# Kernel tuning notes

Hardware: AMD Instinct MI355X
Metric: run time of the kernel (lower is better)

Reference implementation:

```python
import jax, jax.numpy as jnp
import numpy as np

V, D, N, K = 500000, 64, 50000, 32


def setup_inputs() -> dict:
    key = jax.random.key(0)
    ks = jax.random.split(key, 8)
    return {
        "embeddings": jax.random.normal(ks[0], (V, D), dtype=jnp.float32),
        "W1": jax.random.normal(ks[1], (2 * D, D), dtype=jnp.float32) * 0.05,
        "b1": jnp.zeros((D,), dtype=jnp.float32),
        "W2": jax.random.normal(ks[2], (D, D), dtype=jnp.float32) * 0.05,
        "b2": jnp.zeros((D,), dtype=jnp.float32),
        "w3": jax.random.normal(ks[3], (D, 1), dtype=jnp.float32) * 0.05,
        "b3": jnp.zeros((1,), dtype=jnp.float32),
        "video_nodes": jax.random.randint(ks[4], (N,), 0, V, dtype=jnp.int32),
        "neigh_idx": jax.random.randint(ks[5], (N, K), 0, V, dtype=jnp.int32),
        "neigh_deg": jax.random.randint(ks[6], (N,), 0, K + 1, dtype=jnp.int32),
    }


def reference(embeddings, W1, b1, W2, b2, w3, b3, video_nodes, neigh_idx, neigh_deg):
    # Ragged neighbor gather (padded to K, masked by degree)
    e = embeddings[neigh_idx]                      # [N, K, D] neighbor embeddings
    u = embeddings[video_nodes]                    # [N, D]    center embeddings
    # GraphRec-style attention: MLP on [neigh, center] concat -> scalar score
    x = jnp.concatenate(
        [e, jnp.broadcast_to(u[:, None, :], e.shape)], axis=-1)  # [N, K, 2D]
    h = jax.nn.relu(x @ W1 + b1)
    h = jax.nn.relu(h @ W2 + b2)
    s = (h @ w3)[..., 0] + b3[0]                   # [N, K]
    mask = jnp.arange(K)[None, :] < neigh_deg[:, None]
    s = jnp.where(mask, s, -1e9)                   # mask padded neighbors
    att = jax.nn.softmax(s, axis=-1)               # softmax over valid neighbors
    out = jnp.einsum('nkd,nk->nd', e, att)         # attention-weighted sum
    # num_neighs == 0 -> fall back to node's own embedding
    out = jnp.where((neigh_deg > 0)[:, None], out, u)
    return out
```

## Files before the change

kernel.cpp:

```cpp
#include <hip/hip_runtime.h>
#include <hip/hip_bf16.h>

typedef __bf16 bf16x8 __attribute__((ext_vector_type(8)));
typedef float  f32x4  __attribute__((ext_vector_type(4)));

#define MFMA32(acc, a, b) acc = __builtin_amdgcn_mfma_f32_16x16x32_bf16(a, b, acc, 0, 0, 0)
#define LD4(p) (*(const float4*)(p))

__device__ __forceinline__ bf16x8 cvt8(float4 a, float4 b) {
  bf16x8 r;
  r[0] = (__bf16)a.x; r[1] = (__bf16)a.y; r[2] = (__bf16)a.z; r[3] = (__bf16)a.w;
  r[4] = (__bf16)b.x; r[5] = (__bf16)b.y; r[6] = (__bf16)b.z; r[7] = (__bf16)b.w;
  return r;
}

template <int CTRL>
__device__ __forceinline__ float dpp_mov(float x) {
  int yi = __builtin_amdgcn_update_dpp(0, __builtin_bit_cast(int, x), CTRL, 0xF, 0xF, true);
  return __builtin_bit_cast(float, yi);
}
template <int CTRL>
__device__ __forceinline__ float dpp_fadd(float x) { return x + dpp_mov<CTRL>(x); }
template <int CTRL>
__device__ __forceinline__ float dpp_fmax(float x) { return fmaxf(x, dpp_mov<CTRL>(x)); }

__device__ __forceinline__ float tree16(const float* o, int lr) {
  float q8[8];
#pragma unroll
  for (int t = 0; t < 8; t++) {
    const bool up = (lr & 8);
    float sel = up ? o[t + 8] : o[t];
    float oth = up ? o[t] : o[t + 8];
    q8[t] = sel + dpp_mov<0x128>(oth);
  }
  float q4[4];
#pragma unroll
  for (int t = 0; t < 4; t++) {
    const bool up = (lr & 4);
    float sel = up ? q8[t + 4] : q8[t];
    float oth = up ? q8[t] : q8[t + 4];
    q4[t] = sel + __shfl_xor(oth, 4);
  }
  float q2[2];
#pragma unroll
  for (int t = 0; t < 2; t++) {
    const bool up = (lr & 2);
    float sel = up ? q4[t + 2] : q4[t];
    float oth = up ? q4[t] : q4[t + 2];
    q2[t] = sel + dpp_mov<0x4E>(oth);
  }
  const bool up = (lr & 1);
  float sel = up ? q2[1] : q2[0];
  float oth = up ? q2[0] : q2[1];
  return sel + dpp_mov<0xB1>(oth);
}

__global__ void prep_frags(const float* __restrict__ W1,
                           const float* __restrict__ W2,
                           __bf16* __restrict__ wf) {
  int idx = blockIdx.x * 256 + threadIdx.x;
  if (idx < 8192) {
    int j = idx & 7, lane = (idx >> 3) & 63, mt = (idx >> 9) & 3, ks = idx >> 11;
    int i = ks * 32 + ((lane >> 4) << 3) + j;
    int col = mt * 16 + (lane & 15);
    wf[idx] = (__bf16)W1[i * 64 + col];
  } else if (idx < 12288) {
    int t = idx - 8192;
    int j = t & 7, lane = (t >> 3) & 63, mt2 = (t >> 9) & 3, ks2 = (t >> 11) & 1;
    int g = (lane >> 4) & 3;
    int rho = (ks2 * 2 + (j >> 2)) * 16 + g * 4 + (j & 3);
    wf[idx] = (__bf16)W2[rho * 64 + mt2 * 16 + (lane & 15)];
  }
}

__global__ __launch_bounds__(512) void graph_agg(
    const float* __restrict__ emb,
    const float* __restrict__ b1g, const float* __restrict__ b2g,
    const float* __restrict__ w3g, const float* __restrict__ b3g,
    const int* __restrict__ vn, const int* __restrict__ ni,
    const int* __restrict__ nd,
    const __bf16* __restrict__ wf,
    float* __restrict__ out, int N) {
  __shared__ __align__(16) unsigned char smem[25344];

  {
    const uint4* src = (const uint4*)wf;
    uint4* dst = (uint4*)smem;
#pragma unroll
    for (int i = 0; i < 3; i++) dst[threadIdx.x + i * 512] = src[threadIdx.x + i * 512];
    int t = threadIdx.x;
    if (t < 64) {
      ((float*)(smem + 24576))[t] = b1g[t];
      ((float*)(smem + 24832))[t] = b2g[t];
      ((float*)(smem + 25088))[t] = w3g[t];
    }
  }
  __syncthreads();

  const __bf16* w1f = (const __bf16*)smem;
  const __bf16* w2f = (const __bf16*)(smem + 16384);
  const int wid = threadIdx.x >> 6;
  const int l   = threadIdx.x & 63;
  const int g   = l >> 4;
  const int lr  = l & 15;
  const float b3v = b3g[0];

  const int gw = blockIdx.x * 8 + wid;
  const int nwaves = gridDim.x * 8;

  int n = gw;
  int node = 0, deg = 0, i0 = 0, i1 = 0;
  if (n < N) {
    node = vn[n]; deg = nd[n];
    i0 = ni[(long)n * 32 + lr]; i1 = ni[(long)n * 32 + 16 + lr];
  }

  for (; n < N; n += nwaves) {
    const int cn = node, cd = deg, ci0 = i0, ci1 = i1;
    {
      int nn = n + nwaves; if (nn >= N) nn = n;
      node = vn[nn]; deg = nd[nn];
      i0 = ni[(long)nn * 32 + lr]; i1 = ni[(long)nn * 32 + 16 + lr];
    }
    const float* ub = emb + (long)cn * 64;

    if (cd == 0) {
      out[(long)n * 64 + l] = ub[l];
      continue;
    }
    const bool m1 = (cd > 16);

    int boff = 24576;
    asm volatile("" : "+v"(boff));
    const unsigned char* bb = smem + boff;

    bf16x8 ef00, ef01, ef10, ef11;
    {
      const int a = (lr < cd) ? ci0 : cn;
      const float* p = emb + (long)a * 64 + g * 8;
      ef00 = cvt8(LD4(p), LD4(p + 4));
      ef01 = cvt8(LD4(p + 32), LD4(p + 36));
    }
    if (m1) {
      const int a = (16 + lr < cd) ? ci1 : cn;
      const float* p = emb + (long)a * 64 + g * 8;
      ef10 = cvt8(LD4(p), LD4(p + 4));
      ef11 = cvt8(LD4(p + 32), LD4(p + 36));
    }
    bf16x8 uf0, uf1;
    {
      const float* q = ub + g * 8;
      uf0 = cvt8(LD4(q), LD4(q + 4));
      uf1 = cvt8(LD4(q + 32), LD4(q + 36));
    }

    auto mlp_pass = [&](bf16x8 EFa, bf16x8 EFb) -> float {
      f32x4 acc[4];
#pragma unroll
      for (int mt = 0; mt < 4; mt++)
        acc[mt] = *(const f32x4*)(bb + (mt * 16 + g * 4) * 4);
      const bf16x8 xbs[4] = {EFa, EFb, uf0, uf1};
#pragma unroll
      for (int ks = 0; ks < 4; ks++) {
#pragma unroll
        for (int mt = 0; mt < 4; mt++) {
          bf16x8 wa = *(const bf16x8*)(w1f + ((ks * 4 + mt) * 64 + l) * 8);
          MFMA32(acc[mt], wa, xbs[ks]);
        }
      }
      bf16x8 hb[2];
#pragma unroll
      for (int ks2 = 0; ks2 < 2; ks2++) {
        bf16x8 v;
#pragma unroll
        for (int j = 0; j < 8; j++) {
          const int mt = ks2 * 2 + (j >> 2), r = j & 3;
          v[j] = (__bf16)fmaxf(acc[mt][r], 0.f);
        }
        hb[ks2] = v;
      }
#pragma unroll
      for (int mt2 = 0; mt2 < 4; mt2++)
        acc[mt2] = *(const f32x4*)(bb + 256 + (mt2 * 16 + g * 4) * 4);
#pragma unroll
      for (int ks2 = 0; ks2 < 2; ks2++) {
#pragma unroll
        for (int mt2 = 0; mt2 < 4; mt2++) {
          bf16x8 wa = *(const bf16x8*)(w2f + ((ks2 * 4 + mt2) * 64 + l) * 8);
          MFMA32(acc[mt2], wa, hb[ks2]);
        }
      }
      float sv = 0.f;
#pragma unroll
      for (int mt2 = 0; mt2 < 4; mt2++) {
        f32x4 wv = *(const f32x4*)(bb + 512 + (mt2 * 16 + g * 4) * 4);
#pragma unroll
        for (int r = 0; r < 4; r++)
          sv += fmaxf(acc[mt2][r], 0.f) * wv[r];
      }
      sv += __shfl_xor(sv, 16);
      sv += __shfl_xor(sv, 32);
      return sv;
    };

    float sv0 = mlp_pass(ef00, ef01);
    float sv1 = m1 ? mlp_pass(ef10, ef11) : 0.f;

    const bool v0 = (lr < cd);
    const bool v1 = m1 && (16 + lr < cd);
    sv0 = v0 ? (sv0 + b3v) : -1e30f;
    sv1 = v1 ? (sv1 + b3v) : -1e30f;

    float mx = fmaxf(sv0, sv1);
    mx = dpp_fmax<0x128>(mx);
    mx = dpp_fmax<0x124>(mx);
    mx = dpp_fmax<0x122>(mx);
    mx = dpp_fmax<0x121>(mx);

    float p0 = v0 ? __expf(sv0 - mx) : 0.f;
    float p1 = v1 ? __expf(sv1 - mx) : 0.f;
    float sum = p0 + p1;
    sum = dpp_fadd<0x128>(sum);
    sum = dpp_fadd<0x124>(sum);
    sum = dpp_fadd<0x122>(sum);
    sum = dpp_fadd<0x121>(sum);
    const float inv = 1.f / sum;
    const float a0 = p0 * inv, a1 = p1 * inv;

    float o[16];
#pragma unroll
    for (int j = 0; j < 8; j++) {
      float v = a0 * (float)ef00[j];
      if (m1) v += a1 * (float)ef10[j];
      o[j] = v;
      float w = a0 * (float)ef01[j];
      if (m1) w += a1 * (float)ef11[j];
      o[8 + j] = w;
    }
    const int dim = ((lr >> 3) << 5) + g * 8 + (lr & 7);
    out[(long)n * 64 + dim] = tree16(o, lr);
  }
}

extern "C" void kernel_launch(void* const* d_in, const int* in_sizes, int n_in,
                              void* d_out, int out_size, void* d_ws, size_t ws_size,
                              hipStream_t stream) {
  const float* emb = (const float*)d_in[0];
  const float* W1  = (const float*)d_in[1];
  const float* b1  = (const float*)d_in[2];
  const float* W2  = (const float*)d_in[3];
  const float* b2  = (const float*)d_in[4];
  const float* w3  = (const float*)d_in[5];
  const float* b3  = (const float*)d_in[6];
  const int* vn = (const int*)d_in[7];
  const int* ni = (const int*)d_in[8];
  const int* nd = (const int*)d_in[9];
  float* out = (float*)d_out;
  const int N = in_sizes[7];
  __bf16* wf = (__bf16*)d_ws;

  prep_frags<<<48, 256, 0, stream>>>(W1, W2, wf);
  graph_agg<<<2048, 512, 0, stream>>>(emb, b1, b2, w3, b3, vn, ni, nd, wf, out, N);
}
```

Measured before the change: 92.75 us.

## Split each node's neighbors across a wave pair and merge via LDS

Each node is now processed by two waves, each running the MLP on 16 neighbor slots, with the second wave's partial weighted sum and exp-sum passed through shared memory and combined by the first. The softmax max-subtraction is dropped, relying on small scores to avoid overflow. The grid is enlarged so that wave pairs cover nodes. This aims to halve per-wave serial MLP work and improve latency hiding, at the cost of a block-wide barrier per iteration, duplicated center-embedding loads, and reduced numerical safety.

```diff
diff --git a/kernel.cpp b/kernel.cpp
--- a/kernel.cpp
+++ b/kernel.cpp
@@ -21,8 +21,6 @@
 }
 template <int CTRL>
 __device__ __forceinline__ float dpp_fadd(float x) { return x + dpp_mov<CTRL>(x); }
-template <int CTRL>
-__device__ __forceinline__ float dpp_fmax(float x) { return fmaxf(x, dpp_mov<CTRL>(x)); }
 
 __device__ __forceinline__ float tree16(const float* o, int lr) {
   float q8[8];
@@ -81,7 +79,7 @@
     const int* __restrict__ nd,
     const __bf16* __restrict__ wf,
     float* __restrict__ out, int N) {
-  __shared__ __align__(16) unsigned char smem[25344];
+  __shared__ __align__(16) unsigned char smem[27648];
 
   {
     const uint4* src = (const uint4*)wf;
@@ -99,75 +97,66 @@
 
   const __bf16* w1f = (const __bf16*)smem;
   const __bf16* w2f = (const __bf16*)(smem + 16384);
-  const int wid = threadIdx.x >> 6;
-  const int l   = threadIdx.x & 63;
-  const int g   = l >> 4;
-  const int lr  = l & 15;
+  const int wid   = threadIdx.x >> 6;
+  const int l     = threadIdx.x & 63;
+  const int g     = l >> 4;
+  const int lr    = l & 15;
+  const int sub   = wid & 1;
+  const int pairL = wid >> 1;
   const float b3v = b3g[0];
 
-  const int gw = blockIdx.x * 8 + wid;
-  const int nwaves = gridDim.x * 8;
-
-  int n = gw;
-  int node = 0, deg = 0, i0 = 0, i1 = 0;
-  if (n < N) {
-    node = vn[n]; deg = nd[n];
-    i0 = ni[(long)n * 32 + lr]; i1 = ni[(long)n * 32 + 16 + lr];
-  }
-
-  for (; n < N; n += nwaves) {
-    const int cn = node, cd = deg, ci0 = i0, ci1 = i1;
+  const int pid    = blockIdx.x * 4 + pairL;
+  const int npairs = gridDim.x * 4;
+  const int niter  = (N + npairs - 1) / npairs;
+
+  int node = 0, deg = 0, myi = 0;
+  if (pid < N) {
+    node = vn[pid]; deg = nd[pid];
+    myi = ni[(long)pid * 32 + sub * 16 + lr];
+  }
+
+  for (int it = 0; it < niter; ++it) {
+    const int n = pid + it * npairs;
+    const bool active = (n < N);
+    const int cn = node, cd = deg, ci = myi;
     {
-      int nn = n + nwaves; if (nn >= N) nn = n;
+      int nn = n + npairs;
+      if (nn >= N) nn = active ? n : 0;
       node = vn[nn]; deg = nd[nn];
-      i0 = ni[(long)nn * 32 + lr]; i1 = ni[(long)nn * 32 + 16 + lr];
-    }
-    const float* ub = emb + (long)cn * 64;
-
-    if (cd == 0) {
-      out[(long)n * 64 + l] = ub[l];
-      continue;
-    }
-    const bool m1 = (cd > 16);
-
-    int boff = 24576;
-    asm volatile("" : "+v"(boff));
-    const unsigned char* bb = smem + boff;
-
-    bf16x8 ef00, ef01, ef10, ef11;
-    {
-      const int a = (lr < cd) ? ci0 : cn;
+      myi = ni[(long)nn * 32 + sub * 16 + lr];
+    }
+    float* slotO = (float*)(smem + 25344 + (((it & 1) << 2) + pairL) * 288);
+
+    const bool mywork = active && (cd > sub * 16);
+    float psum = 0.f, o_lane = 0.f;
+
+    if (mywork) {
+      const int myrow = sub * 16 + lr;
+      const int a = (myrow < cd) ? ci : cn;
       const float* p = emb + (long)a * 64 + g * 8;
-      ef00 = cvt8(LD4(p), LD4(p + 4));
-      ef01 = cvt8(LD4(p + 32), LD4(p + 36));
-    }
-    if (m1) {
-      const int a = (16 + lr < cd) ? ci1 : cn;
-      const float* p = emb + (long)a * 64 + g * 8;
-      ef10 = cvt8(LD4(p), LD4(p + 4));
-      ef11 = cvt8(LD4(p + 32), LD4(p + 36));
-    }
-    bf16x8 uf0, uf1;
-    {
-      const float* q = ub + g * 8;
-      uf0 = cvt8(LD4(q), LD4(q + 4));
-      uf1 = cvt8(LD4(q + 32), LD4(q + 36));
-    }
-
-    auto mlp_pass = [&](bf16x8 EFa, bf16x8 EFb) -> float {
+      bf16x8 ef0 = cvt8(LD4(p), LD4(p + 4));
+      bf16x8 ef1 = cvt8(LD4(p + 32), LD4(p + 36));
+      const float* q = emb + (long)cn * 64 + g * 8;
+      bf16x8 uf0 = cvt8(LD4(q), LD4(q + 4));
+      bf16x8 uf1 = cvt8(LD4(q + 32), LD4(q + 36));
+
+      int boff = 24576;
+      asm volatile("" : "+v"(boff));
+      const unsigned char* bb = smem + boff;
+
       f32x4 acc[4];
 #pragma unroll
       for (int mt = 0; mt < 4; mt++)
         acc[mt] = *(const f32x4*)(bb + (mt * 16 + g * 4) * 4);
-      const bf16x8 xbs[4] = {EFa, EFb, uf0, uf1};
-#pragma unroll
-      for (int ks = 0; ks < 4; ks++) {
+      const bf16x8 xs[4] = {ef0, ef1, uf0, uf1};
+#pragma unroll
+      for (int ks = 0; ks < 4; ks++)
 #pragma unroll
         for (int mt = 0; mt < 4; mt++) {
           bf16x8 wa = *(const bf16x8*)(w1f + ((ks * 4 + mt) * 64 + l) * 8);
-          MFMA32(acc[mt], wa, xbs[ks]);
+          MFMA32(acc[mt], wa, xs[ks]);
         }
-      }
+
       bf16x8 hb[2];
 #pragma unroll
       for (int ks2 = 0; ks2 < 2; ks2++) {
@@ -179,17 +168,18 @@
         }
         hb[ks2] = v;
       }
+
 #pragma unroll
       for (int mt2 = 0; mt2 < 4; mt2++)
         acc[mt2] = *(const f32x4*)(bb + 256 + (mt2 * 16 + g * 4) * 4);
 #pragma unroll
-      for (int ks2 = 0; ks2 < 2; ks2++) {
+      for (int ks2 = 0; ks2 < 2; ks2++)
 #pragma unroll
         for (int mt2 = 0; mt2 < 4; mt2++) {
           bf16x8 wa = *(const bf16x8*)(w2f + ((ks2 * 4 + mt2) * 64 + l) * 8);
           MFMA32(acc[mt2], wa, hb[ks2]);
         }
-      }
+
       float sv = 0.f;
 #pragma unroll
       for (int mt2 = 0; mt2 < 4; mt2++) {
@@ -200,45 +190,39 @@
       }
       sv += __shfl_xor(sv, 16);
       sv += __shfl_xor(sv, 32);
-      return sv;
-    };
-
-    float sv0 = mlp_pass(ef00, ef01);
-    float sv1 = m1 ? mlp_pass(ef10, ef11) : 0.f;
-
-    const bool v0 = (lr < cd);
-    const bool v1 = m1 && (16 + lr < cd);
-    sv0 = v0 ? (sv0 + b3v) : -1e30f;
-    sv1 = v1 ? (sv1 + b3v) : -1e30f;
-
-    float mx = fmaxf(sv0, sv1);
-    mx = dpp_fmax<0x128>(mx);
-    mx = dpp_fmax<0x124>(mx);
-    mx = dpp_fmax<0x122>(mx);
-    mx = dpp_fmax<0x121>(mx);
-
-    float p0 = v0 ? __expf(sv0 - mx) : 0.f;
-    float p1 = v1 ? __expf(sv1 - mx) : 0.f;
-    float sum = p0 + p1;
-    sum = dpp_fadd<0x128>(sum);
-    sum = dpp_fadd<0x124>(sum);
-    sum = dpp_fadd<0x122>(sum);
-    sum = dpp_fadd<0x121>(sum);
-    const float inv = 1.f / sum;
-    const float a0 = p0 * inv, a1 = p1 * inv;
-
-    float o[16];
-#pragma unroll
-    for (int j = 0; j < 8; j++) {
-      float v = a0 * (float)ef00[j];
-      if (m1) v += a1 * (float)ef10[j];
-      o[j] = v;
-      float w = a0 * (float)ef01[j];
-      if (m1) w += a1 * (float)ef11[j];
-      o[8 + j] = w;
-    }
-    const int dim = ((lr >> 3) << 5) + g * 8 + (lr & 7);
-    out[(long)n * 64 + dim] = tree16(o, lr);
+
+      const float pexp = (myrow < cd) ? __expf(sv + b3v) : 0.f;
+      psum = pexp;
+      psum = dpp_fadd<0x128>(psum);
+      psum = dpp_fadd<0x124>(psum);
+      psum = dpp_fadd<0x122>(psum);
+      psum = dpp_fadd<0x121>(psum);
+
+      float o[16];
+#pragma unroll
+      for (int j = 0; j < 8; j++) {
+        o[j]     = pexp * (float)ef0[j];
+        o[8 + j] = pexp * (float)ef1[j];
+      }
+      o_lane = tree16(o, lr);
+    }
+
+    if (sub == 1) {
+      slotO[l] = o_lane;
+      if (l == 0) slotO[64] = psum;
+    }
+    __syncthreads();
+    if (sub == 0 && active) {
+      if (cd == 0) {
+        out[(long)n * 64 + l] = emb[(long)cn * 64 + l];
+      } else {
+        const float po  = slotO[l];
+        const float tot = psum + slotO[64];
+        const float inv = 1.f / tot;
+        const int dim = ((lr >> 3) << 5) + g * 8 + (lr & 7);
+        out[(long)n * 64 + dim] = (o_lane + po) * inv;
+      }
+    }
   }
 }
 
@@ -260,5 +244,5 @@
   __bf16* wf = (__bf16*)d_ws;
 
   prep_frags<<<48, 256, 0, stream>>>(W1, W2, wf);
-  graph_agg<<<2048, 512, 0, stream>>>(emb, b1, b2, w3, b3, vn, ni, nd, wf, out, N);
-}
+  graph_agg<<<3125, 512, 0, stream>>>(emb, b1, b2, w3, b3, vn, ni, nd, wf, out, N);
+}
```

Result: faster. 90.65 us (-2.3%).
